# Performance work log

Measured on AMD Instinct MI355X. Metric: run time of the kernel, lower is better.

The kernel has to match this reference:

```python
import jax, jax.numpy as jnp
import numpy as np

B, TQ, TK = 4, 1024, 1024
D, H, DFF = 1024, 16, 4096
DH = D // H
EPS = 1e-6  # added to sigma (std), not variance, per the torch LayerNorm


def layer_norm(x, g, b):
    mu = jnp.mean(x, axis=-1, keepdims=True)
    sigma = jnp.sqrt(jnp.mean((x - mu) ** 2, axis=-1, keepdims=True))  # unbiased=False
    return (x - mu) / (sigma + EPS) * g + b


def mha(q_in, k_in, v_in, mask, wq, bq, wk, bk, wv, bv, wo, bo):
    # q_in: [B,Tq,D], k_in/v_in: [B,Tk,D], mask: [B,Tq,Tk] bool (True = masked)
    b, tq, _ = q_in.shape
    tk = k_in.shape[1]
    q = (q_in @ wq + bq).reshape(b, tq, H, DH).transpose(0, 2, 1, 3)  # [B,H,Tq,DH]
    k = (k_in @ wk + bk).reshape(b, tk, H, DH).transpose(0, 2, 1, 3)  # [B,H,Tk,DH]
    v = (v_in @ wv + bv).reshape(b, tk, H, DH).transpose(0, 2, 1, 3)  # [B,H,Tk,DH]
    logits = jnp.einsum('bhqd,bhkd->bhqk', q, k) / np.float32(np.sqrt(DH))
    logits = jnp.where(mask[:, None, :, :], -jnp.inf, logits)  # broadcast over heads
    attn = jax.nn.softmax(logits, axis=-1)
    out = jnp.einsum('bhqk,bhkd->bhqd', attn, v)  # [B,H,Tq,DH]
    out = out.transpose(0, 2, 1, 3).reshape(b, tq, D)  # [B,Tq,D]
    return out @ wo + bo


def setup_inputs() -> dict:
    key = jax.random.key(0)
    ks = jax.random.split(key, 32)
    s = 0.02
    def lin(i, din, dout):
        return (jax.random.normal(ks[i], (din, dout), jnp.float32) * s,
                jnp.zeros((dout,), jnp.float32))
    inp = {}
    inp['x'] = jax.random.normal(ks[0], (B, TQ, D), jnp.float32)
    inp['src_x'] = jax.random.normal(ks[1], (B, TK, D), jnp.float32)
    causal = jnp.triu(jnp.ones((TQ, TQ), jnp.bool_), k=1)
    inp['mask'] = jnp.broadcast_to(causal, (B, TQ, TQ))
    inp['src_mask'] = jnp.zeros((B, TQ, TK), jnp.bool_)
    for j, (g, bname) in enumerate([('ln1_g', 'ln1_b'), ('ln2_g', 'ln2_b'), ('ln3_g', 'ln3_b')]):
        inp[g] = jnp.ones((D,), jnp.float32)
        inp[bname] = jnp.zeros((D,), jnp.float32)
    names = ['sa_wq', 'sa_wk', 'sa_wv', 'sa_wo', 'ca_wq', 'ca_wk', 'ca_wv', 'ca_wo']
    for j, n in enumerate(names):
        w, bb = lin(2 + j, D, D)
        inp[n] = w
        inp[n.replace('w', 'b', 1).replace('_b', '_b')] = bb
        inp[n[:3] + 'b' + n[4]] = bb
    # clean bias naming
    for n in names:
        inp.pop(n[:3] + 'b' + n[4], None)
        inp.pop(n.replace('w', 'b', 1), None)
    for j, n in enumerate(names):
        w, bb = lin(2 + j, D, D)
        inp[n] = w
        inp['b' + n] = bb
    w1, b1 = lin(12, D, DFF)
    w2, b2 = lin(13, DFF, D)
    inp['ff_w1'], inp['ff_b1'], inp['ff_w2'], inp['ff_b2'] = w1, b1, w2, b2
    return inp


def reference(x, src_x, mask, src_mask,
              ln1_g, ln1_b, ln2_g, ln2_b, ln3_g, ln3_b,
              sa_wq, bsa_wq, sa_wk, bsa_wk, sa_wv, bsa_wv, sa_wo, bsa_wo,
              ca_wq, bca_wq, ca_wk, bca_wk, ca_wv, bca_wv, ca_wo, bca_wo,
              ff_w1, ff_b1, ff_w2, ff_b2):
    # pre-layer-norm decoder layer (dropout=0 / eval mode)
    h = layer_norm(x, ln1_g, ln1_b)
    x1 = x + mha(h, h, h, mask, sa_wq, bsa_wq, sa_wk, bsa_wk, sa_wv, bsa_wv, sa_wo, bsa_wo)
    h2 = layer_norm(x1, ln2_g, ln2_b)
    x2 = x1 + mha(h2, src_x, src_x, src_mask, ca_wq, bca_wq, ca_wk, bca_wk, ca_wv, bca_wv, ca_wo, bca_wo)
    h3 = layer_norm(x2, ln3_g, ln3_b)
    ff = jax.nn.relu(h3 @ ff_w1 + ff_b1) @ ff_w2 + ff_b2
    return x2 + ff
```

## Files before the change

### kernel.cpp

```cpp
#include <hip/hip_runtime.h>

typedef __bf16 bf16;
typedef __attribute__((ext_vector_type(8))) __bf16 bf16x8;
typedef __attribute__((ext_vector_type(4))) __bf16 bf16x4;
typedef __attribute__((ext_vector_type(4))) float f32x4;

#define MFMA16(a, b, c) __builtin_amdgcn_mfma_f32_16x16x32_bf16((a), (b), (c), 0, 0, 0)

static const long MMe = 1L << 20;
#define QSCALE_F 0.18033688011112042f

__device__ __forceinline__ void async_cp16(void* lds, const void* g) {
    __builtin_amdgcn_global_load_lds((__attribute__((address_space(1))) void*)g,
                                     (__attribute__((address_space(3))) void*)lds, 16, 0, 0);
}

__device__ __forceinline__ void ln_body(const float* __restrict__ x,
                                        const float* __restrict__ g,
                                        const float* __restrict__ b,
                                        bf16* __restrict__ out,
                                        long row, int tid,
                                        float* red1, float* red2)
{
    const int wave = tid >> 6, lane = tid & 63;

    f32x4 v = *(const f32x4*)(x + row * 1024 + tid * 4);
    float s = v[0] + v[1] + v[2] + v[3];
    for (int off = 32; off > 0; off >>= 1) s += __shfl_xor(s, off, 64);
    if (lane == 0) red1[wave] = s;
    __syncthreads();
    const float mu = (red1[0] + red1[1] + red1[2] + red1[3]) * (1.f / 1024.f);

    float s2 = 0.f;
    for (int i = 0; i < 4; ++i) { float d = v[i] - mu; s2 += d * d; }
    for (int off = 32; off > 0; off >>= 1) s2 += __shfl_xor(s2, off, 64);
    if (lane == 0) red2[wave] = s2;
    __syncthreads();
    const float var = (red2[0] + red2[1] + red2[2] + red2[3]) * (1.f / 1024.f);
    const float inv = 1.f / (sqrtf(var) + 1e-6f);

    f32x4 gv = *(const f32x4*)(g + tid * 4);
    f32x4 bv = *(const f32x4*)(b + tid * 4);
    bf16x4 ov;
    for (int i = 0; i < 4; ++i)
        ov[i] = (bf16)((v[i] - mu) * inv * gv[i] + bv[i]);
    *(bf16x4*)(out + row * 1024 + tid * 4) = ov;
}

__global__ __launch_bounds__(256) void ln_k(const float* __restrict__ x,
                                            const float* __restrict__ g,
                                            const float* __restrict__ b,
                                            bf16* __restrict__ out)
{
    __shared__ float red1[4];
    __shared__ float red2[4];
    ln_body(x, g, b, out, blockIdx.x, threadIdx.x, red1, red2);
}

__device__ __forceinline__ void transpose_body(const float* __restrict__ in,
                                               bf16* __restrict__ out,
                                               int R, int C, int bx, int by,
                                               int tid, bf16 (*t)[33])
{
    const int r = tid >> 5, c = tid & 31;
    for (int i = 0; i < 4; ++i)
        t[r + i * 8][c] = (bf16)in[(long)(by + r + i * 8) * C + bx + c];
    __syncthreads();
    for (int i = 0; i < 4; ++i)
        out[(long)(bx + r + i * 8) * R + by + c] = t[c][r + i * 8];
}

__global__ __launch_bounds__(256) void prep_k(
    const float* i0, const float* i1, const float* i2, const float* i3,
    const float* i4, const float* i5, const float* i6, const float* i7,
    bf16* WT_SA,
    const float* ff_w1, bf16* WT_F1,
    const float* ff_w2, bf16* WT_F2,
    const float* src_x, bf16* SrcB,
    const float* x, const float* ln1_g, const float* ln1_b, bf16* Hbuf)
{
    __shared__ bf16 t[32][33];
    __shared__ float red1[4];
    __shared__ float red2[4];
    const int tid = threadIdx.x;
    const long b = blockIdx.x;

    if (b < 8192) {
        const int iz = (int)(b >> 10), w = (int)(b & 1023);
        const float* in;
        switch (iz) {
            case 0: in = i0; break; case 1: in = i1; break;
            case 2: in = i2; break; case 3: in = i3; break;
            case 4: in = i4; break; case 5: in = i5; break;
            case 6: in = i6; break; default: in = i7; break;
        }
        bf16* out = WT_SA + ((long)iz << 20);
        transpose_body(in, out, 1024, 1024, (w & 31) * 32, (w >> 5) * 32, tid, t);
    } else if (b < 12288) {
        const int w = (int)(b - 8192);
        transpose_body(ff_w1, WT_F1, 1024, 4096, (w & 127) * 32, (w >> 7) * 32, tid, t);
    } else if (b < 16384) {
        const int w = (int)(b - 12288);
        transpose_body(ff_w2, WT_F2, 4096, 1024, (w & 31) * 32, (w >> 5) * 32, tid, t);
    } else if (b < 20480) {
        const long i = (b - 16384) * 1024 + tid * 4;
        f32x4 v = *(const f32x4*)(src_x + i);
        bf16x4 o;
        for (int j = 0; j < 4; ++j) o[j] = (bf16)v[j];
        *(bf16x4*)(SrcB + i) = o;
    } else {
        ln_body(x, ln1_g, ln1_b, Hbuf, b - 20480, tid, red1, red2);
    }
}

template <int BM, int BN, int STORE, bool BIAS, bool RELU, bool RES, bool OUTF32, bool SPLIT, bool QS, bool DUALA, int PX>
__global__ __launch_bounds__(256) void gemm_k(const bf16* __restrict__ A,
                                              const bf16* __restrict__ A2,
                                              int lda,
                                              const bf16* __restrict__ Bt, int ldb,
                                              const float* __restrict__ bias,
                                              const float* __restrict__ bias2,
                                              const float* __restrict__ bias3,
                                              const float* __restrict__ res,
                                              void* __restrict__ Cv,
                                              void* __restrict__ Cv2,
                                              int M, int N, int K)
{
    constexpr int MI = BM / 32, NI = BN / 32;
    __shared__ __align__(16) bf16 As[BM * 64];
    __shared__ __align__(16) bf16 Bs[BN * 64];
    const int tid  = threadIdx.x;
    const int wave = tid >> 6, lane = tid & 63;
    const int quad = lane >> 4, l15 = lane & 15;
    const int wm = wave >> 1, wn = wave & 1;

    int tx, ty, tz;
    if (PX > 0) {
        const unsigned wgid = (blockIdx.z * gridDim.y + blockIdx.y) * gridDim.x + blockIdx.x;
        const int xcd = wgid & 7, lid = wgid >> 3;
        const int npx = gridDim.x / PX;
        const int PY  = (gridDim.y * gridDim.z) / (8 / npx);
        const int ix  = lid % PX, iyz = lid / PX;
        const int pxi = xcd % npx, pyi = xcd / npx;
        const int tyz = pyi * PY + iyz;
        tx = pxi * PX + ix;
        ty = tyz % gridDim.y;
        tz = tyz / gridDim.y;
    } else {
        tx = blockIdx.x; ty = blockIdx.y; tz = blockIdx.z;
    }

    const long m0 = (long)ty * BM;
    const long n0 = (long)tx * BN;
    const long kbase = SPLIT ? (long)tz * K : 0;

    const bf16* Abase = A;
    if (DUALA && (n0 >> 10) >= 1) Abase = A2;

    f32x4 acc[MI][NI];
    for (int i = 0; i < MI; ++i)
        for (int j = 0; j < NI; ++j)
            acc[i][j] = (f32x4){0.f, 0.f, 0.f, 0.f};

    const int lr = lane >> 3;
    const int lc = (((lane & 7) ^ (lr & 7)) * 8);
    const bf16* Ag = Abase + (m0 + lr) * (long)lda + lc + kbase;
    const bf16* Bg = Bt    + (n0 + lr) * (long)ldb + lc + kbase;

    for (int k0 = 0; k0 < K; k0 += 64) {
        __syncthreads();
        for (int s = wave; s < BM / 8; s += 4)
            async_cp16(&As[s * 512], Ag + (long)(s * 8) * lda + k0);
        for (int s = wave; s < BN / 8; s += 4)
            async_cp16(&Bs[s * 512], Bg + (long)(s * 8) * ldb + k0);
        __syncthreads();
        for (int kk = 0; kk < 2; ++kk) {
            bf16x8 af[MI], bfr[NI];
            for (int i = 0; i < MI; ++i) {
                const int row = wm * (BM / 2) + i * 16 + l15;
                af[i]  = *(const bf16x8*)&As[row * 64 + (((kk * 4 + quad) ^ (l15 & 7)) * 8)];
            }
            for (int j = 0; j < NI; ++j) {
                const int row = wn * (BN / 2) + j * 16 + l15;
                bfr[j] = *(const bf16x8*)&Bs[row * 64 + (((kk * 4 + quad) ^ (l15 & 7)) * 8)];
            }
            for (int mi = 0; mi < MI; ++mi)
                for (int ni = 0; ni < NI; ++ni)
                    acc[mi][ni] = MFMA16(af[mi], bfr[ni], acc[mi][ni]);
        }
    }

    float* outp = (float*)Cv;
    if (SPLIT && tz) outp = (float*)Cv2;

    for (int ni = 0; ni < NI; ++ni) {
        const int col = (int)n0 + wn * (BN / 2) + ni * 16 + l15;
        float bv = 0.f;
        int which = 0, c1 = col;
        if (STORE == 3) {
            which = col >> 10; c1 = col & 1023;
            if (BIAS) bv = (which == 0 ? bias : (which == 1 ? bias2 : bias3))[c1];
        } else if (STORE == 4) {
            which = col >> 10; c1 = col & 1023;
            if (BIAS) bv = (which ? bias2 : bias)[c1];
        } else if (BIAS) {
            bv = bias[col];
        }
        for (int mi = 0; mi < MI; ++mi) {
            for (int r = 0; r < 4; ++r) {
                const int row = (int)m0 + wm * (BM / 2) + mi * 16 + quad * 4 + r;
                float v = acc[mi][ni][r] + bv;
                if (QS && (STORE == 1 || (STORE == 3 && which == 0))) v *= QSCALE_F;
                if (RES)  v += res[(long)row * N + col];
                if (RELU) v = v > 0.f ? v : 0.f;
                long oidx;
                if (STORE == 0) {
                    oidx = (long)row * N + col;
                } else {
                    const int bb = row >> 10, t = row & 1023;
                    const int hh = c1 >> 6,  dh = c1 & 63;
                    const long qidx = ((long)(bb * 16 + hh) * 1024 + t) * 64 + dh;
                    const long vidx = ((long)(bb * 16 + hh) * 64 + dh) * 1024 + t;
                    if (STORE == 1)      oidx = qidx;
                    else if (STORE == 2) oidx = vidx;
                    else if (STORE == 3) oidx = (which == 2) ? (8 * MMe + vidx)
                                                             : ((long)which * 4 * MMe + qidx);
                    else                 oidx = which ? (4 * MMe + vidx) : qidx;
                }
                if (OUTF32) outp[oidx] = v;
                else        ((bf16*)Cv)[oidx] = (bf16)v;
            }
        }
    }
}

__global__ __launch_bounds__(256) void red2_k(const float* __restrict__ P0,
                                              const float* __restrict__ P1,
                                              const float* __restrict__ bias,
                                              const float* __restrict__ res,
                                              float* __restrict__ out)
{
    const long i = (long)blockIdx.x * 1024 + threadIdx.x * 4;
    f32x4 a = *(const f32x4*)(P0 + i);
    f32x4 b = *(const f32x4*)(P1 + i);
    f32x4 r = *(const f32x4*)(res + i);
    f32x4 bv = *(const f32x4*)(bias + threadIdx.x * 4);
    f32x4 o;
    for (int j = 0; j < 4; ++j) o[j] = a[j] + b[j] + r[j] + bv[j];
    *(f32x4*)(out + i) = o;
}

__device__ __forceinline__ void attn_tile(const bf16x8* aq,
                                          const bf16* Ks, const bf16* Vs, bf16* Psw,
                                          int tk0, int q0w, int quad, int l15, int l7,
                                          bool domask, f32x4* o, float* rs)
{
    f32x4 s[8];
    for (int ct = 0; ct < 8; ++ct) {
        f32x4 sv = (f32x4){0.f, 0.f, 0.f, 0.f};
        sv = MFMA16(aq[0], *(const bf16x8*)&Ks[(ct * 16 + l15) * 64 + ((quad ^ l7) * 8)], sv);
        sv = MFMA16(aq[1], *(const bf16x8*)&Ks[(ct * 16 + l15) * 64 + (((4 + quad) ^ l7) * 8)], sv);
        s[ct] = sv;
    }
    if (domask) {
        for (int ct = 0; ct < 8; ++ct) {
            const int cg = tk0 + ct * 16 + l15;
            for (int r = 0; r < 4; ++r)
                if (cg > q0w + quad * 4 + r) s[ct][r] = -1e30f;
        }
    }
    for (int ct = 0; ct < 8; ++ct) {
        for (int r = 0; r < 4; ++r) {
            const float p = exp2f(s[ct][r]);
            rs[r] += p;
            Psw[(quad * 4 + r) * 136 + ct * 16 + l15] = (bf16)p;
        }
    }
    for (int kk = 0; kk < 4; ++kk) {
        const bf16x8 ap = *(const bf16x8*)&Psw[l15 * 136 + kk * 32 + quad * 8];
        for (int nt = 0; nt < 4; ++nt) {
            const bf16x8 bv = *(const bf16x8*)&Vs[(nt * 16 + l15) * 128 + (((kk * 4 + quad) ^ l15) * 8)];
            o[nt] = MFMA16(ap, bv, o[nt]);
        }
    }
}

__global__ __launch_bounds__(256) void attn_causal_k(const bf16* __restrict__ Q,
                                                     const bf16* __restrict__ K,
                                                     const bf16* __restrict__ Vt,
                                                     bf16* __restrict__ Out)
{
    __shared__ __align__(16) bf16 Ks[128 * 64];
    __shared__ __align__(16) bf16 Vs[64 * 128];
    __shared__ __align__(16) bf16 Ps[4][16 * 136];

    const int tid  = threadIdx.x;
    const int wave = tid >> 6, lane = tid & 63;
    const int quad = lane >> 4, l15 = lane & 15, l7 = l15 & 7;
    const int x  = blockIdx.x;
    const int bh = blockIdx.y;
    const int hh = bh & 15, bb = bh >> 4;

    const bf16* Qp = Q  + (long)bh * 1024 * 64;
    const bf16* Kp = K  + (long)bh * 1024 * 64;
    const bf16* Vp = Vt + (long)bh * 64 * 1024;

    const int qA = x, qB = 15 - x;
    const int q0A = qA * 64 + wave * 16, q0B = qB * 64 + wave * 16;
    const int chA = qA >> 1, chB = qB >> 1;

    bf16x8 aqA[2], aqB[2];
    aqA[0] = *(const bf16x8*)&Qp[(q0A + l15) * 64 + quad * 8];
    aqA[1] = *(const bf16x8*)&Qp[(q0A + l15) * 64 + quad * 8 + 32];
    aqB[0] = *(const bf16x8*)&Qp[(q0B + l15) * 64 + quad * 8];
    aqB[1] = *(const bf16x8*)&Qp[(q0B + l15) * 64 + quad * 8 + 32];

    f32x4 oA[4], oB[4];
    float rsA[4] = {0.f, 0.f, 0.f, 0.f}, rsB[4] = {0.f, 0.f, 0.f, 0.f};
    for (int nt = 0; nt < 4; ++nt) {
        oA[nt] = (f32x4){0.f, 0.f, 0.f, 0.f};
        oB[nt] = (f32x4){0.f, 0.f, 0.f, 0.f};
    }

    const int krow = lane >> 3;
    const int kcol = (((lane & 7) ^ (krow & 7)) * 8);
    const int vrow = lane >> 4;

    for (int ch = 0; ch <= chB; ++ch) {
        const int tk0 = ch * 128;
        __syncthreads();
        for (int s = wave; s < 16; s += 4)
            async_cp16(&Ks[s * 512], &Kp[(long)(tk0 + s * 8 + krow) * 64 + kcol]);
        for (int s = wave; s < 16; s += 4) {
            const int row = s * 4 + vrow;
            const int vcol = ((l15 ^ (row & 15)) * 8);
            async_cp16(&Vs[s * 512], &Vp[(long)row * 1024 + tk0 + vcol]);
        }
        __syncthreads();
        if (ch <= chA)
            attn_tile(aqA, Ks, Vs, Ps[wave], tk0, q0A, quad, l15, l7, ch == chA, oA, rsA);
        attn_tile(aqB, Ks, Vs, Ps[wave], tk0, q0B, quad, l15, l7, ch == chB, oB, rsB);
    }

    for (int r = 0; r < 4; ++r) {
        for (int off = 1; off < 16; off <<= 1) {
            rsA[r] += __shfl_xor(rsA[r], off, 64);
            rsB[r] += __shfl_xor(rsB[r], off, 64);
        }
    }
    for (int nt = 0; nt < 4; ++nt) {
        for (int r = 0; r < 4; ++r) {
            const int col = hh * 64 + nt * 16 + l15;
            Out[((long)bb * 1024 + q0A + quad * 4 + r) * 1024 + col] = (bf16)(oA[nt][r] / rsA[r]);
            Out[((long)bb * 1024 + q0B + quad * 4 + r) * 1024 + col] = (bf16)(oB[nt][r] / rsB[r]);
        }
    }
}

__global__ __launch_bounds__(256) void attn_cross_k(const bf16* __restrict__ Q,
                                                    const bf16* __restrict__ K,
                                                    const bf16* __restrict__ Vt,
                                                    bf16* __restrict__ Out)
{
    __shared__ __align__(16) bf16 Ks[128 * 64];
    __shared__ __align__(16) bf16 Vs[64 * 128];
    __shared__ __align__(16) bf16 Ps[4][16 * 136];

    const int tid  = threadIdx.x;
    const int wave = tid >> 6, lane = tid & 63;
    const int quad = lane >> 4, l15 = lane & 15, l7 = l15 & 7;
    const int qb = blockIdx.x;
    const int bh = blockIdx.y;
    const int hh = bh & 15, bb = bh >> 4;

    const bf16* Qp = Q  + (long)bh * 1024 * 64;
    const bf16* Kp = K  + (long)bh * 1024 * 64;
    const bf16* Vp = Vt + (long)bh * 64 * 1024;
    const int q0w = qb * 64 + wave * 16;

    bf16x8 aq[2];
    aq[0] = *(const bf16x8*)&Qp[(q0w + l15) * 64 + quad * 8];
    aq[1] = *(const bf16x8*)&Qp[(q0w + l15) * 64 + quad * 8 + 32];

    f32x4 o[4];
    float rs[4] = {0.f, 0.f, 0.f, 0.f};
    for (int nt = 0; nt < 4; ++nt) o[nt] = (f32x4){0.f, 0.f, 0.f, 0.f};

    const int krow = lane >> 3;
    const int kcol = (((lane & 7) ^ (krow & 7)) * 8);
    const int vrow = lane >> 4;

    for (int ch = 0; ch < 8; ++ch) {
        const int tk0 = ch * 128;
        __syncthreads();
        for (int s = wave; s < 16; s += 4)
            async_cp16(&Ks[s * 512], &Kp[(long)(tk0 + s * 8 + krow) * 64 + kcol]);
        for (int s = wave; s < 16; s += 4) {
            const int row = s * 4 + vrow;
            const int vcol = ((l15 ^ (row & 15)) * 8);
            async_cp16(&Vs[s * 512], &Vp[(long)row * 1024 + tk0 + vcol]);
        }
        __syncthreads();
        attn_tile(aq, Ks, Vs, Ps[wave], tk0, q0w, quad, l15, l7, false, o, rs);
    }

    for (int r = 0; r < 4; ++r)
        for (int off = 1; off < 16; off <<= 1) rs[r] += __shfl_xor(rs[r], off, 64);

    for (int nt = 0; nt < 4; ++nt) {
        for (int r = 0; r < 4; ++r) {
            const int t   = q0w + quad * 4 + r;
            const int col = hh * 64 + nt * 16 + l15;
            Out[((long)bb * 1024 + t) * 1024 + col] = (bf16)(o[nt][r] / rs[r]);
        }
    }
}

extern "C" void kernel_launch(void* const* d_in, const int* in_sizes, int n_in,
                              void* d_out, int out_size, void* d_ws, size_t ws_size,
                              hipStream_t stream)
{
    const float* x     = (const float*)d_in[0];
    const float* src_x = (const float*)d_in[1];
    const float* ln1_g = (const float*)d_in[4];
    const float* ln1_b = (const float*)d_in[5];
    const float* ln2_g = (const float*)d_in[6];
    const float* ln2_b = (const float*)d_in[7];
    const float* ln3_g = (const float*)d_in[8];
    const float* ln3_b = (const float*)d_in[9];
    const float* sa_wq = (const float*)d_in[10];
    const float* sa_wk = (const float*)d_in[11];
    const float* sa_wv = (const float*)d_in[12];
    const float* sa_wo = (const float*)d_in[13];
    const float* ca_wq = (const float*)d_in[14];
    const float* ca_wk = (const float*)d_in[15];
    const float* ca_wv = (const float*)d_in[16];
    const float* ca_wo = (const float*)d_in[17];
    const float* bsa_wq = (const float*)d_in[18];
    const float* bsa_wk = (const float*)d_in[19];
    const float* bsa_wv = (const float*)d_in[20];
    const float* bsa_wo = (const float*)d_in[21];
    const float* bca_wq = (const float*)d_in[22];
    const float* bca_wk = (const float*)d_in[23];
    const float* bca_wv = (const float*)d_in[24];
    const float* bca_wo = (const float*)d_in[25];
    const float* ff_w1 = (const float*)d_in[26];
    const float* ff_b1 = (const float*)d_in[27];
    const float* ff_w2 = (const float*)d_in[28];
    const float* ff_b2 = (const float*)d_in[29];

    bf16* ws = (bf16*)d_ws;
    bf16*  WT_SA = ws;
    bf16*  WT_CA = ws + 4 * MMe;
    bf16*  WT_F1 = ws + 8 * MMe;
    bf16*  WT_F2 = ws + 12 * MMe;
    bf16*  Hbuf  = ws + 16 * MMe;
    bf16*  SrcB  = ws + 20 * MMe;
    bf16*  Qb    = ws + 24 * MMe;
    bf16*  Kb    = ws + 28 * MMe;
    bf16*  Vtb   = ws + 32 * MMe;
    bf16*  Attn  = ws + 36 * MMe;
    float* X1    = (float*)(ws + 40 * MMe);
    bf16*  FF1   = ws + 24 * MMe;
    float* P0    = (float*)ws;
    float* P1    = (float*)(ws + 16 * MMe);
    float* X2    = (float*)d_out;

    const dim3 blk(256);

    prep_k<<<24576, blk, 0, stream>>>(sa_wq, sa_wk, sa_wv, sa_wo,
                                      ca_wq, ca_wk, ca_wv, ca_wo, WT_SA,
                                      ff_w1, WT_F1, ff_w2, WT_F2,
                                      src_x, SrcB,
                                      x, ln1_g, ln1_b, Hbuf);

    gemm_k<128, 128, 3, true, false, false, false, false, true, false, 6><<<dim3(24, 32), blk, 0, stream>>>(
        Hbuf, nullptr, 1024, WT_SA, 1024, bsa_wq, bsa_wk, bsa_wv, nullptr, Qb, nullptr, 4096, 3072, 1024);
    attn_causal_k<<<dim3(8, 64), blk, 0, stream>>>(Qb, Kb, Vtb, Attn);
    gemm_k<64, 64, 0, true, false, true, true, false, false, false, 8><<<dim3(16, 64), blk, 0, stream>>>(
        Attn, nullptr, 1024, WT_SA + 3 * MMe, 1024, bsa_wo, nullptr, nullptr, x, X1, nullptr, 4096, 1024, 1024);

    ln_k<<<4096, blk, 0, stream>>>(X1, ln2_g, ln2_b, Hbuf);
    gemm_k<128, 128, 3, true, false, false, false, false, true, true, 6><<<dim3(24, 32), blk, 0, stream>>>(
        Hbuf, SrcB, 1024, WT_CA, 1024, bca_wq, bca_wk, bca_wv, nullptr, Qb, nullptr, 4096, 3072, 1024);
    attn_cross_k<<<dim3(16, 64), blk, 0, stream>>>(Qb, Kb, Vtb, Attn);
    gemm_k<64, 64, 0, true, false, true, true, false, false, false, 8><<<dim3(16, 64), blk, 0, stream>>>(
        Attn, nullptr, 1024, WT_CA + 3 * MMe, 1024, bca_wo, nullptr, nullptr, X1, X2, nullptr, 4096, 1024, 1024);

    ln_k<<<4096, blk, 0, stream>>>(X2, ln3_g, ln3_b, Hbuf);
    gemm_k<128, 128, 0, true, true, false, false, false, false, false, 8><<<dim3(32, 32), blk, 0, stream>>>(
        Hbuf, nullptr, 1024, WT_F1, 1024, ff_b1, nullptr, nullptr, nullptr, FF1, nullptr, 4096, 4096, 1024);
    gemm_k<128, 128, 0, false, false, false, true, true, false, false, 8><<<dim3(8, 32, 2), blk, 0, stream>>>(
        FF1, nullptr, 4096, WT_F2, 4096, nullptr, nullptr, nullptr, nullptr, P0, P1, 4096, 1024, 2048);
    red2_k<<<4096, blk, 0, stream>>>(P0, P1, ff_b2, X2, (float*)d_out);

    (void)in_sizes; (void)n_in; (void)out_size; (void)ws_size;
}
```

Measured before the change: 502.3 us.

## Read K and V fragments directly from global memory in attention kernels

Both attention kernels stop staging K and V tiles into shared memory with async copies and block-wide barriers. Each wave now loads its MFMA operands straight from global memory, with no swizzle, relying on the cache for reuse across the four waves. This removes the LDS traffic and the two __syncthreads per chunk, and frees LDS for higher occupancy. In exchange every wave issues its own global loads, so L2/L1 traffic rises and load latency sits directly in front of the MFMAs.

```diff
diff --git a/kernel.cpp b/kernel.cpp
--- a/kernel.cpp
+++ b/kernel.cpp
@@ -250,16 +250,19 @@
     *(f32x4*)(out + i) = o;
 }
 
-__device__ __forceinline__ void attn_tile(const bf16x8* aq,
-                                          const bf16* Ks, const bf16* Vs, bf16* Psw,
-                                          int tk0, int q0w, int quad, int l15, int l7,
-                                          bool domask, f32x4* o, float* rs)
+__device__ __forceinline__ void attn_tile_g(const bf16x8* aq,
+                                            const bf16* __restrict__ Kp,
+                                            const bf16* __restrict__ Vp,
+                                            bf16* Psw,
+                                            int tk0, int q0w, int quad, int l15,
+                                            bool domask, f32x4* o, float* rs)
 {
     f32x4 s[8];
     for (int ct = 0; ct < 8; ++ct) {
         f32x4 sv = (f32x4){0.f, 0.f, 0.f, 0.f};
-        sv = MFMA16(aq[0], *(const bf16x8*)&Ks[(ct * 16 + l15) * 64 + ((quad ^ l7) * 8)], sv);
-        sv = MFMA16(aq[1], *(const bf16x8*)&Ks[(ct * 16 + l15) * 64 + (((4 + quad) ^ l7) * 8)], sv);
+        const bf16* kr = Kp + (long)(tk0 + ct * 16 + l15) * 64 + quad * 8;
+        sv = MFMA16(aq[0], *(const bf16x8*)(kr), sv);
+        sv = MFMA16(aq[1], *(const bf16x8*)(kr + 32), sv);
         s[ct] = sv;
     }
     if (domask) {
@@ -279,7 +282,7 @@
     for (int kk = 0; kk < 4; ++kk) {
         const bf16x8 ap = *(const bf16x8*)&Psw[l15 * 136 + kk * 32 + quad * 8];
         for (int nt = 0; nt < 4; ++nt) {
-            const bf16x8 bv = *(const bf16x8*)&Vs[(nt * 16 + l15) * 128 + (((kk * 4 + quad) ^ l15) * 8)];
+            const bf16x8 bv = *(const bf16x8*)(Vp + (long)(nt * 16 + l15) * 1024 + tk0 + (kk * 4 + quad) * 8);
             o[nt] = MFMA16(ap, bv, o[nt]);
         }
     }
@@ -290,13 +293,11 @@
                                                      const bf16* __restrict__ Vt,
                                                      bf16* __restrict__ Out)
 {
-    __shared__ __align__(16) bf16 Ks[128 * 64];
-    __shared__ __align__(16) bf16 Vs[64 * 128];
     __shared__ __align__(16) bf16 Ps[4][16 * 136];
 
     const int tid  = threadIdx.x;
     const int wave = tid >> 6, lane = tid & 63;
-    const int quad = lane >> 4, l15 = lane & 15, l7 = l15 & 7;
+    const int quad = lane >> 4, l15 = lane & 15;
     const int x  = blockIdx.x;
     const int bh = blockIdx.y;
     const int hh = bh & 15, bb = bh >> 4;
@@ -322,24 +323,11 @@
         oB[nt] = (f32x4){0.f, 0.f, 0.f, 0.f};
     }
 
-    const int krow = lane >> 3;
-    const int kcol = (((lane & 7) ^ (krow & 7)) * 8);
-    const int vrow = lane >> 4;
-
     for (int ch = 0; ch <= chB; ++ch) {
         const int tk0 = ch * 128;
-        __syncthreads();
-        for (int s = wave; s < 16; s += 4)
-            async_cp16(&Ks[s * 512], &Kp[(long)(tk0 + s * 8 + krow) * 64 + kcol]);
-        for (int s = wave; s < 16; s += 4) {
-            const int row = s * 4 + vrow;
-            const int vcol = ((l15 ^ (row & 15)) * 8);
-            async_cp16(&Vs[s * 512], &Vp[(long)row * 1024 + tk0 + vcol]);
-        }
-        __syncthreads();
         if (ch <= chA)
-            attn_tile(aqA, Ks, Vs, Ps[wave], tk0, q0A, quad, l15, l7, ch == chA, oA, rsA);
-        attn_tile(aqB, Ks, Vs, Ps[wave], tk0, q0B, quad, l15, l7, ch == chB, oB, rsB);
+            attn_tile_g(aqA, Kp, Vp, Ps[wave], tk0, q0A, quad, l15, ch == chA, oA, rsA);
+        attn_tile_g(aqB, Kp, Vp, Ps[wave], tk0, q0B, quad, l15, ch == chB, oB, rsB);
     }
 
     for (int r = 0; r < 4; ++r) {
@@ -362,13 +350,11 @@
                                                     const bf16* __restrict__ Vt,
                                                     bf16* __restrict__ Out)
 {
-    __shared__ __align__(16) bf16 Ks[128 * 64];
-    __shared__ __align__(16) bf16 Vs[64 * 128];
     __shared__ __align__(16) bf16 Ps[4][16 * 136];
 
     const int tid  = threadIdx.x;
     const int wave = tid >> 6, lane = tid & 63;
-    const int quad = lane >> 4, l15 = lane & 15, l7 = l15 & 7;
+    const int quad = lane >> 4, l15 = lane & 15;
     const int qb = blockIdx.x;
     const int bh = blockIdx.y;
     const int hh = bh & 15, bb = bh >> 4;
@@ -386,22 +372,9 @@
     float rs[4] = {0.f, 0.f, 0.f, 0.f};
     for (int nt = 0; nt < 4; ++nt) o[nt] = (f32x4){0.f, 0.f, 0.f, 0.f};
 
-    const int krow = lane >> 3;
-    const int kcol = (((lane & 7) ^ (krow & 7)) * 8);
-    const int vrow = lane >> 4;
-
     for (int ch = 0; ch < 8; ++ch) {
         const int tk0 = ch * 128;
-        __syncthreads();
-        for (int s = wave; s < 16; s += 4)
-            async_cp16(&Ks[s * 512], &Kp[(long)(tk0 + s * 8 + krow) * 64 + kcol]);
-        for (int s = wave; s < 16; s += 4) {
-            const int row = s * 4 + vrow;
-            const int vcol = ((l15 ^ (row & 15)) * 8);
-            async_cp16(&Vs[s * 512], &Vp[(long)row * 1024 + tk0 + vcol]);
-        }
-        __syncthreads();
-        attn_tile(aq, Ks, Vs, Ps[wave], tk0, q0w, quad, l15, l7, false, o, rs);
+        attn_tile_g(aq, Kp, Vp, Ps[wave], tk0, q0w, quad, l15, false, o, rs);
     }
 
     for (int r = 0; r < 4; ++r)
```

Measured after the change: 634.8 us. 1.26x slower.
